# Kernel optimization log

Hardware: AMD Instinct MI355X
Metric: run time of the kernel (lower is better)

Reference implementation:

```python
import jax, jax.numpy as jnp
import numpy as np


def setup_inputs() -> dict:
    key = jax.random.key(0)
    k1, k2 = jax.random.split(key)
    B, S, D = 4, 8192, 1024
    x = jax.random.normal(k1, (B, S, D), dtype=jnp.float32)
    alpha = jax.random.uniform(k2, (B, S, D), dtype=jnp.float32)
    return {"x": x, "alpha": alpha}


def reference(x, alpha):
    # Linear recurrence h_t = alpha_t * h_{t-1} + x_t, computed as an
    # associative scan over the sequence axis (axis=1).
    def linear_combine(i, j):
        x_i, a_i = i
        x_j, a_j = j
        return (a_j * x_i + x_j, a_j * a_i)

    ys, _ = jax.lax.associative_scan(linear_combine, (x, alpha), axis=1)
    return ys
```

## Files before the change

kernel.cpp:

```cpp
#include <hip/hip_runtime.h>

constexpr int B  = 4;
constexpr int S  = 8192;
constexpr int D  = 1024;
constexpr int C  = 128;
constexpr int L  = S / C;
constexpr int D4 = D / 4;

__global__ __launch_bounds__(256) void phase1(const float4* __restrict__ x,
                                              const float4* __restrict__ a,
                                              float4* __restrict__ Xagg,
                                              float4* __restrict__ Aagg) {
    const int t = threadIdx.x;
    const int c = blockIdx.x;
    const int b = blockIdx.y;
    long base = ((long)(b * S + c * L)) * D4 + t;

    float4 X = {0.f, 0.f, 0.f, 0.f};
    float4 A = {1.f, 1.f, 1.f, 1.f};
    #pragma unroll 8
    for (int s = 0; s < L; ++s) {
        float4 xv = x[base + (long)s * D4];
        float4 av = a[base + (long)s * D4];
        X.x = fmaf(av.x, X.x, xv.x);
        X.y = fmaf(av.y, X.y, xv.y);
        X.z = fmaf(av.z, X.z, xv.z);
        X.w = fmaf(av.w, X.w, xv.w);
        A.x *= av.x; A.y *= av.y; A.z *= av.z; A.w *= av.w;
    }
    long o = ((long)(b * C + c)) * D4 + t;
    Xagg[o] = X;
    Aagg[o] = A;
}

__global__ __launch_bounds__(256) void phase2(float* __restrict__ Xagg,
                                              const float* __restrict__ Aagg) {
    const int g = blockIdx.x * blockDim.x + threadIdx.x;
    const int b = g / D;
    const int d = g % D;
    long base = (long)b * C * D + d;
    float carry = 0.f;
    for (int c = 0; c < C; ++c) {
        long o = base + (long)c * D;
        float X = Xagg[o];
        float A = Aagg[o];
        Xagg[o] = carry;
        carry = fmaf(A, carry, X);
    }
}

__global__ __launch_bounds__(256) void phase3(const float4* __restrict__ x,
                                              const float4* __restrict__ a,
                                              const float4* __restrict__ prefix,
                                              float4* __restrict__ out) {
    const int t = threadIdx.x;
    const int c = blockIdx.x;
    const int b = blockIdx.y;

    float4 h = prefix[((long)(b * C + c)) * D4 + t];
    long base = ((long)(b * S + c * L)) * D4 + t;
    #pragma unroll 8
    for (int s = 0; s < L; ++s) {
        float4 xv = x[base + (long)s * D4];
        float4 av = a[base + (long)s * D4];
        h.x = fmaf(av.x, h.x, xv.x);
        h.y = fmaf(av.y, h.y, xv.y);
        h.z = fmaf(av.z, h.z, xv.z);
        h.w = fmaf(av.w, h.w, xv.w);
        out[base + (long)s * D4] = h;
    }
}

extern "C" void kernel_launch(void* const* d_in, const int* in_sizes, int n_in,
                              void* d_out, int out_size, void* d_ws, size_t ws_size,
                              hipStream_t stream) {
    const float4* x = (const float4*)d_in[0];
    const float4* a = (const float4*)d_in[1];
    float4* out = (float4*)d_out;

    float* Xagg = (float*)d_ws;
    float* Aagg = Xagg + (size_t)B * C * D;

    dim3 grid1(C, B);
    phase1<<<grid1, 256, 0, stream>>>(x, a, (float4*)Xagg, (float4*)Aagg);

    phase2<<<(B * D) / 256, 256, 0, stream>>>(Xagg, Aagg);

    phase3<<<grid1, 256, 0, stream>>>(x, a, (const float4*)Xagg, out);
}
```

Measured before the change: 372.9 us.

## Increase chunk count, shrink phase2 blocks, add nontemporal output stores

Raises the chunk count from 128 to 512 so phases 1 and 3 launch 2048 blocks instead of 512, giving more parallelism across the GPU's compute units. Phase 2 moves to 64-thread blocks with a 4-way unrolled serial loop that batches loads. Phase 3 writes its output with nontemporal stores so the output does not pollute the cache. The costs are a longer serial carry chain in phase 2 (512 steps) and four times larger aggregate arrays.

```diff
diff --git a/kernel.cpp b/kernel.cpp
--- a/kernel.cpp
+++ b/kernel.cpp
@@ -3,22 +3,24 @@
 constexpr int B  = 4;
 constexpr int S  = 8192;
 constexpr int D  = 1024;
-constexpr int C  = 128;
+constexpr int C  = 512;
 constexpr int L  = S / C;
 constexpr int D4 = D / 4;
 
-__global__ __launch_bounds__(256) void phase1(const float4* __restrict__ x,
-                                              const float4* __restrict__ a,
-                                              float4* __restrict__ Xagg,
-                                              float4* __restrict__ Aagg) {
+typedef float nt_float4 __attribute__((ext_vector_type(4)));
+
+__global__ __launch_bounds__(256, 8) void phase1(const float4* __restrict__ x,
+                                                 const float4* __restrict__ a,
+                                                 float4* __restrict__ Xagg,
+                                                 float4* __restrict__ Aagg) {
     const int t = threadIdx.x;
     const int c = blockIdx.x;
     const int b = blockIdx.y;
-    long base = ((long)(b * S + c * L)) * D4 + t;
+    const long base = ((long)(b * S + c * L)) * D4 + t;
 
     float4 X = {0.f, 0.f, 0.f, 0.f};
     float4 A = {1.f, 1.f, 1.f, 1.f};
-    #pragma unroll 8
+    #pragma unroll 4
     for (int s = 0; s < L; ++s) {
         float4 xv = x[base + (long)s * D4];
         float4 av = a[base + (long)s * D4];
@@ -28,38 +30,42 @@
         X.w = fmaf(av.w, X.w, xv.w);
         A.x *= av.x; A.y *= av.y; A.z *= av.z; A.w *= av.w;
     }
-    long o = ((long)(b * C + c)) * D4 + t;
+    const long o = ((long)(b * C + c)) * D4 + t;
     Xagg[o] = X;
     Aagg[o] = A;
 }
 
-__global__ __launch_bounds__(256) void phase2(float* __restrict__ Xagg,
-                                              const float* __restrict__ Aagg) {
-    const int g = blockIdx.x * blockDim.x + threadIdx.x;
-    const int b = g / D;
-    const int d = g % D;
-    long base = (long)b * C * D + d;
+__global__ __launch_bounds__(64) void phase2(float* __restrict__ Xagg,
+                                             const float* __restrict__ Aagg) {
+    const int g = blockIdx.x * 64 + threadIdx.x;
+    const int b = g >> 10;
+    const int d = g & (D - 1);
+    float*       Xp = Xagg + (long)b * C * D + d;
+    const float* Ap = Aagg + (long)b * C * D + d;
     float carry = 0.f;
-    for (int c = 0; c < C; ++c) {
-        long o = base + (long)c * D;
-        float X = Xagg[o];
-        float A = Aagg[o];
-        Xagg[o] = carry;
-        carry = fmaf(A, carry, X);
+    for (int c = 0; c < C; c += 4) {
+        const long o0 = (long)c * D, o1 = o0 + D, o2 = o1 + D, o3 = o2 + D;
+        const float X0 = Xp[o0], X1 = Xp[o1], X2 = Xp[o2], X3 = Xp[o3];
+        const float A0 = Ap[o0], A1 = Ap[o1], A2 = Ap[o2], A3 = Ap[o3];
+        Xp[o0] = carry; carry = fmaf(A0, carry, X0);
+        Xp[o1] = carry; carry = fmaf(A1, carry, X1);
+        Xp[o2] = carry; carry = fmaf(A2, carry, X2);
+        Xp[o3] = carry; carry = fmaf(A3, carry, X3);
     }
 }
 
-__global__ __launch_bounds__(256) void phase3(const float4* __restrict__ x,
-                                              const float4* __restrict__ a,
-                                              const float4* __restrict__ prefix,
-                                              float4* __restrict__ out) {
+__global__ __launch_bounds__(256, 8) void phase3(const float4* __restrict__ x,
+                                                 const float4* __restrict__ a,
+                                                 const float4* __restrict__ prefix,
+                                                 float4* __restrict__ out) {
     const int t = threadIdx.x;
     const int c = blockIdx.x;
     const int b = blockIdx.y;
 
     float4 h = prefix[((long)(b * C + c)) * D4 + t];
-    long base = ((long)(b * S + c * L)) * D4 + t;
-    #pragma unroll 8
+    const long base = ((long)(b * S + c * L)) * D4 + t;
+    nt_float4* ntout = (nt_float4*)out;
+    #pragma unroll 4
     for (int s = 0; s < L; ++s) {
         float4 xv = x[base + (long)s * D4];
         float4 av = a[base + (long)s * D4];
@@ -67,7 +73,8 @@
         h.y = fmaf(av.y, h.y, xv.y);
         h.z = fmaf(av.z, h.z, xv.z);
         h.w = fmaf(av.w, h.w, xv.w);
-        out[base + (long)s * D4] = h;
+        nt_float4 hv = {h.x, h.y, h.z, h.w};
+        __builtin_nontemporal_store(hv, &ntout[base + (long)s * D4]);
     }
 }
 
@@ -84,7 +91,7 @@
     dim3 grid1(C, B);
     phase1<<<grid1, 256, 0, stream>>>(x, a, (float4*)Xagg, (float4*)Aagg);
 
-    phase2<<<(B * D) / 256, 256, 0, stream>>>(Xagg, Aagg);
+    phase2<<<(B * D) / 64, 64, 0, stream>>>(Xagg, Aagg);
 
     phase3<<<grid1, 256, 0, stream>>>(x, a, (const float4*)Xagg, out);
 }
```

Result: no change. 374.7 us (+0.5%).
